# Optimization experiments

Measured on AMD Instinct MI355X. Metric: run time of the kernel, lower is better.

Reference implementation:

```python
import jax, jax.numpy as jnp
import numpy as np

NUM_HEADS = 16


def setup_inputs() -> dict:
    key = jax.random.key(0)
    k1, k2, k3 = jax.random.split(key, 3)
    T, B, E = 2048, 2, 1024
    query = jax.random.normal(k1, (T, B, E), dtype=jnp.float32)
    # xavier-uniform-ish init for qkv weight, small normal for output proj
    lim = (6.0 / (3 * E + E)) ** 0.5
    W_qkv = jax.random.uniform(k2, (3 * E, E), dtype=jnp.float32, minval=-lim, maxval=lim)
    W_o = jax.random.normal(k3, (E, E), dtype=jnp.float32) * 0.02
    b_qkv = jnp.zeros((3 * E,), dtype=jnp.float32)
    b_o = jnp.zeros((E,), dtype=jnp.float32)
    return {"query": query, "W_qkv": W_qkv, "b_qkv": b_qkv, "W_o": W_o, "b_o": b_o}


def reference(query, W_qkv, b_qkv, W_o, b_o):
    T, B, E = query.shape
    H = NUM_HEADS
    hd = E // H
    scaling = float(hd) ** -0.5

    # fused qkv projection: [T, B, 3E]
    qkv = jnp.einsum('tbe,fe->tbf', query, W_qkv) + b_qkv
    q, k, v = jnp.split(qkv, 3, axis=-1)
    q = q * scaling

    def to_heads(x):  # [T, B, E] -> [B*H, T, hd]
        return x.reshape(T, B * H, hd).transpose(1, 0, 2)

    q, k, v = to_heads(q), to_heads(k), to_heads(v)

    # explicit bmm QK^T -> softmax -> bmm AV (faithful to source)
    scores = jnp.einsum('bqd,bkd->bqk', q, k)          # [B*H, T, T]
    attn = jax.nn.softmax(scores, axis=-1)             # dropout p=0.0 (eval)
    ctx = jnp.einsum('bqk,bkd->bqd', attn, v)          # [B*H, T, hd]

    out = ctx.transpose(1, 0, 2).reshape(T, B, E)
    out = jnp.einsum('tbe,fe->tbf', out, W_o) + b_o    # o_net

    avg_weights = attn.reshape(B, H, T, T).sum(axis=1) / H  # need_weights=True path
    return out, avg_weights
```

## Files before the change

### kernel.cpp

```cpp
#include <hip/hip_runtime.h>
#include <stdint.h>

typedef unsigned short u16;
typedef __bf16 bf16x8 __attribute__((ext_vector_type(8)));
typedef float f32x4 __attribute__((ext_vector_type(4)));
typedef float f32x16 __attribute__((ext_vector_type(16)));

__device__ __forceinline__ u16 f2b(float f) {
  unsigned u = __builtin_bit_cast(unsigned, f);
  u += 0x7fffu + ((u >> 16) & 1u);
  return (u16)(u >> 16);
}

__device__ __forceinline__ float fexp2(float x) { return __builtin_amdgcn_exp2f(x); }

__device__ __forceinline__ void gld_lds16(const void* g, void* l) {
  __builtin_amdgcn_global_load_lds((const __attribute__((address_space(1))) unsigned int*)g,
                                   (__attribute__((address_space(3))) unsigned int*)l,
                                   16, 0, 0);
}

__global__ __launch_bounds__(256) void k_cvt3(
    const float* __restrict__ s0, u16* __restrict__ d0,
    const float* __restrict__ s1, u16* __restrict__ d1,
    const float* __restrict__ s2, u16* __restrict__ d2) {
  const int bx = blockIdx.x;
  const float* s;
  u16* d;
  int i0;
  if (bx < 4096)      { s = s0; d = d0; i0 = bx; }
  else if (bx < 7168) { s = s1; d = d1; i0 = bx - 4096; }
  else                { s = s2; d = d2; i0 = bx - 7168; }
  const int i = i0 * 256 + threadIdx.x;
  float4 v = reinterpret_cast<const float4*>(s)[i];
  ushort4 o;
  o.x = f2b(v.x); o.y = f2b(v.y); o.z = f2b(v.z); o.w = f2b(v.w);
  reinterpret_cast<ushort4*>(d)[i] = o;
}

template <int EPI>
__device__ __forceinline__ void gemm_body(
    const u16* __restrict__ A, const u16* __restrict__ B, const float* __restrict__ bias,
    float* __restrict__ outF, u16* __restrict__ q_ws, u16* __restrict__ k_ws,
    u16* __restrict__ vt_ws, int tm, int tn, u16* smem) {
  u16* Al0 = smem;
  u16* Bl0 = smem + 8192;
  const int tid = threadIdx.x;
  const int w = tid >> 6, lane = tid & 63;
  const int wr = w >> 1, wc = w & 1;
  const int lo = lane & 15, hi = lane >> 4;
  const size_t arow0 = (size_t)tm * 128;
  const size_t brow0 = (size_t)tn * 128;

  f32x4 acc[4][4] = {};

  const int rr = lane >> 2;
  const int kswz = ((lane & 3) ^ ((rr >> 1) & 3)) * 8;
  const int rsw = (lo >> 1) & 3;

  for (int rs = 0; rs < 2; ++rs) {
    int seg = rs * 4 + w;
    gld_lds16(A + (arow0 + seg * 16 + rr) * 1024 + kswz, &Al0[seg * 512 + lane * 8]);
    gld_lds16(B + (brow0 + seg * 16 + rr) * 1024 + kswz, &Bl0[seg * 512 + lane * 8]);
  }
  __syncthreads();
  int cur = 0;
  for (int kb = 0; kb < 32; ++kb) {
    if (kb + 1 < 32) {
      const int k0 = (kb + 1) * 32 + kswz;
      u16* Ad = Al0 + (cur ^ 1) * 4096;
      u16* Bd = Bl0 + (cur ^ 1) * 4096;
      for (int rs = 0; rs < 2; ++rs) {
        int seg = rs * 4 + w;
        gld_lds16(A + (arow0 + seg * 16 + rr) * 1024 + k0, &Ad[seg * 512 + lane * 8]);
        gld_lds16(B + (brow0 + seg * 16 + rr) * 1024 + k0, &Bd[seg * 512 + lane * 8]);
      }
    }
    const u16* Ac = Al0 + cur * 4096;
    const u16* Bc = Bl0 + cur * 4096;
    bf16x8 af[4], bfr[4];
#pragma unroll
    for (int m = 0; m < 4; ++m)
      af[m] = *(const bf16x8*)&Ac[(wr * 64 + m * 16 + lo) * 32 + ((hi ^ rsw) * 8)];
#pragma unroll
    for (int n = 0; n < 4; ++n)
      bfr[n] = *(const bf16x8*)&Bc[(wc * 64 + n * 16 + lo) * 32 + ((hi ^ rsw) * 8)];
#pragma unroll
    for (int m = 0; m < 4; ++m)
#pragma unroll
      for (int n = 0; n < 4; ++n)
        acc[m][n] = __builtin_amdgcn_mfma_f32_16x16x32_bf16(af[m], bfr[n], acc[m][n], 0, 0, 0);
    __syncthreads();
    cur ^= 1;
  }

  if (EPI == 0) {
#pragma unroll
    for (int n = 0; n < 4; ++n) {
      const int col = tn * 128 + wc * 64 + n * 16 + lo;
      const float bb = bias[col];
#pragma unroll
      for (int m = 0; m < 4; ++m)
#pragma unroll
        for (int r = 0; r < 4; ++r) {
          const int row = tm * 128 + wr * 64 + m * 16 + hi * 4 + r;
          outF[(size_t)row * 1024 + col] = acc[m][n][r] + bb;
        }
    }
  } else {
    const int sec = tn >> 3;
#pragma unroll
    for (int n = 0; n < 4; ++n) {
      const int cin = (tn & 7) * 128 + wc * 64 + n * 16 + lo;
      const int h = cin >> 6, d = cin & 63;
      const float bb = bias[sec * 1024 + cin];
#pragma unroll
      for (int m = 0; m < 4; ++m) {
        const int rowb = tm * 128 + wr * 64 + m * 16 + hi * 4;
        const int t0 = rowb >> 1;
        const float v0 = acc[m][n][0] + bb, v1 = acc[m][n][1] + bb;
        const float v2 = acc[m][n][2] + bb, v3 = acc[m][n][3] + bb;
        if (sec == 0) {
          const float s = 0.18033688f;
          q_ws[(((size_t)h * 2048 + t0) * 64) + d]            = f2b(v0 * s);
          q_ws[(((size_t)(16 + h) * 2048 + t0) * 64) + d]     = f2b(v1 * s);
          q_ws[(((size_t)h * 2048 + t0 + 1) * 64) + d]        = f2b(v2 * s);
          q_ws[(((size_t)(16 + h) * 2048 + t0 + 1) * 64) + d] = f2b(v3 * s);
        } else if (sec == 1) {
          k_ws[(((size_t)h * 2048 + t0) * 64) + d]            = f2b(v0);
          k_ws[(((size_t)(16 + h) * 2048 + t0) * 64) + d]     = f2b(v1);
          k_ws[(((size_t)h * 2048 + t0 + 1) * 64) + d]        = f2b(v2);
          k_ws[(((size_t)(16 + h) * 2048 + t0 + 1) * 64) + d] = f2b(v3);
        } else {
          const int tp0 = (t0 & ~12) | ((t0 & 4) << 1) | ((t0 & 8) >> 1);
          ushort2 p0, p1;
          p0.x = f2b(v0); p0.y = f2b(v2);
          p1.x = f2b(v1); p1.y = f2b(v3);
          *(ushort2*)(vt_ws + ((size_t)h * 64 + d) * 2048 + tp0) = p0;
          *(ushort2*)(vt_ws + ((size_t)(16 + h) * 64 + d) * 2048 + tp0) = p1;
        }
      }
    }
  }
}

__global__ __launch_bounds__(256) void k_gemm_qkv(
    const u16* __restrict__ A, const u16* __restrict__ B, const float* __restrict__ bias,
    u16* __restrict__ q_ws, u16* __restrict__ k_ws, u16* __restrict__ vt_ws) {
  __shared__ __align__(16) u16 smem[16384];
  const int flat = blockIdx.y * 24 + blockIdx.x;
  const int xcd = flat & 7, idx = flat >> 3;
  const int wg = xcd * 96 + idx;
  gemm_body<1>(A, B, bias, nullptr, q_ws, k_ws, vt_ws, wg / 24, wg % 24, smem);
}

__device__ __forceinline__ void avg_body(
    const u16* __restrict__ q_ws, const u16* __restrict__ k_ws,
    const float* __restrict__ c_ws, float* __restrict__ avg,
    int kx, int qy, int b, u16* smem) {
  u16* Kl0 = smem;
  const int tid = threadIdx.x, w = tid >> 6, lane = tid & 63;
  const int lo = lane & 15, hi = lane >> 4;
  const int kbase = kx * 128;
  const int qb = qy * 64;
  const int qrow = qb + w * 16 + lo;
  const int qrow_base = qb + w * 16 + hi * 4;

  const int r0 = tid >> 3, c0 = tid & 7;
  const int ldsoff = r0 * 128 + ((c0 ^ (r0 & 7)) << 4);
  const u16* kg = k_ws + ((size_t)(b * 16) * 2048 + kbase + r0) * 64 + c0 * 8;
  const int l7 = lo & 7;

  float acc[8][4] = {};
  const f32x4 zero = {0.f, 0.f, 0.f, 0.f};

  uint4 rg0 = *(const uint4*)(kg);
  uint4 rg1 = *(const uint4*)(kg + 32 * 64);
  uint4 rg2 = *(const uint4*)(kg + 64 * 64);
  uint4 rg3 = *(const uint4*)(kg + 96 * 64);
  {
    char* dst = (char*)Kl0 + ldsoff;
    *(uint4*)(dst) = rg0;
    *(uint4*)(dst + 32 * 128) = rg1;
    *(uint4*)(dst + 64 * 128) = rg2;
    *(uint4*)(dst + 96 * 128) = rg3;
  }
  __syncthreads();

  int cur = 0;
  for (int h = 0; h < 16; ++h) {
    const int bh = b * 16 + h;
    if (h + 1 < 16) {
      const u16* kgn = kg + (size_t)(h + 1) * 2048 * 64;
      rg0 = *(const uint4*)(kgn);
      rg1 = *(const uint4*)(kgn + 32 * 64);
      rg2 = *(const uint4*)(kgn + 64 * 64);
      rg3 = *(const uint4*)(kgn + 96 * 64);
    }
    const u16* qp = q_ws + ((size_t)bh * 2048 + qrow) * 64 + hi * 8;
    bf16x8 qf0 = *(const bf16x8*)qp;
    bf16x8 qf1 = *(const bf16x8*)(qp + 32);
    const float4 cf = *(const float4*)(c_ws + (size_t)bh * 2048 + qrow_base);
    const float cfa[4] = {cf.x, cf.y, cf.z, cf.w};
    const char* kbse = (const char*)(Kl0 + cur * 8192);
#pragma unroll
    for (int n = 0; n < 8; ++n) {
      const char* kp = kbse + (n * 16 + lo) * 128;
      bf16x8 k0 = *(const bf16x8*)(kp + ((hi ^ l7) << 4));
      bf16x8 k1 = *(const bf16x8*)(kp + (((hi + 4) ^ l7) << 4));
      f32x4 s = __builtin_amdgcn_mfma_f32_16x16x32_bf16(qf0, k0, zero, 0, 0, 0);
      s = __builtin_amdgcn_mfma_f32_16x16x32_bf16(qf1, k1, s, 0, 0, 0);
#pragma unroll
      for (int r = 0; r < 4; ++r) acc[n][r] += fexp2(s[r]) * cfa[r];
    }
    if (h + 1 < 16) {
      char* dst = (char*)(Kl0 + (cur ^ 1) * 8192) + ldsoff;
      *(uint4*)(dst) = rg0;
      *(uint4*)(dst + 32 * 128) = rg1;
      *(uint4*)(dst + 64 * 128) = rg2;
      *(uint4*)(dst + 96 * 128) = rg3;
      __syncthreads();
    }
    cur ^= 1;
  }

  const float s16 = 1.0f / 16.0f;
#pragma unroll
  for (int n = 0; n < 8; ++n)
#pragma unroll
    for (int r = 0; r < 4; ++r)
      avg[((size_t)(b * 2048 + qrow_base + r)) * 2048 + kbase + n * 16 + lo] = acc[n][r] * s16;
}

__global__ __launch_bounds__(256) void k_tail(
    const u16* __restrict__ ctx, const u16* __restrict__ wobf, const float* __restrict__ bo,
    float* __restrict__ out, const u16* __restrict__ q_ws, const u16* __restrict__ k_ws,
    const float* __restrict__ c_ws, float* __restrict__ avg) {
  __shared__ __align__(16) u16 smem[16384];
  const int bx = blockIdx.x;
  if (bx < 256) {
    gemm_body<0>(ctx, wobf, bo, out, nullptr, nullptr, nullptr, bx >> 3, bx & 7, smem);
  } else {
    const int id = bx - 256;
    avg_body(q_ws, k_ws, c_ws, avg, id & 15, (id >> 4) & 31, id >> 9, smem);
  }
}

__global__ __launch_bounds__(1024) void k_flash(
    const u16* __restrict__ q_ws, const u16* __restrict__ k_ws, const u16* __restrict__ vt_ws,
    u16* __restrict__ ctx_ws, float* __restrict__ c_ws) {
  __shared__ __align__(16) u16 KVl[33792];
  const int tid = threadIdx.x, w = tid >> 6, lane = tid & 63;
  const int h = lane >> 5, l31 = lane & 31, l7 = lane & 7;
  const int hh = w >> 3;
  const int wq = w & 7;
  const int tid_h = tid & 511;

  const int flat = blockIdx.y * 8 + blockIdx.x;
  const int xcd = flat & 7, idx = flat >> 3;
  const int bh = xcd * 4 + (idx & 3);
  const int qtile = idx >> 2;
  const int b = bh >> 4, head = bh & 15;
  const int qbase = qtile * 256;
  const int qrow = qbase + wq * 32 + l31;

  bf16x8 qf[4];
#pragma unroll
  for (int j = 0; j < 4; ++j)
    qf[j] = *(const bf16x8*)(q_ws + ((size_t)bh * 2048 + qrow) * 64 + j * 16 + h * 8);

  const int srow = tid_h >> 3, schk = tid_h & 7;
  const int xc = (schk ^ (srow & 7)) * 8;
  const u16* kgA = k_ws + ((size_t)bh * 2048 + hh * 1024 + srow) * 64 + xc;
  const u16* vgA = vt_ws + ((size_t)bh * 64 + srow) * 2048 + hh * 1024 + xc;

  f32x16 ca0 = {}, ca1 = {};
  float lrow = 0.f;

  {
    u16* base = KVl + hh * 8192;
    gld_lds16(kgA, base + tid_h * 8);
    gld_lds16(vgA, base + 4096 + tid_h * 8);
  }
  __syncthreads();

  int cur = 0;
  for (int it = 0; it < 16; ++it) {
    if (it < 15) {
      u16* base = KVl + (cur ^ 1) * 16384 + hh * 8192;
      gld_lds16(kgA + (size_t)(it + 1) * 4096, base + tid_h * 8);
      gld_lds16(vgA + (it + 1) * 64, base + 4096 + tid_h * 8);
    }
    const char* Kb = (const char*)(KVl + cur * 16384 + hh * 8192);
    const char* Vb = Kb + 8192;

    f32x16 st0 = {}, st1 = {};
    __builtin_amdgcn_s_setprio(1);
#pragma unroll
    for (int j = 0; j < 4; ++j) {
      bf16x8 k0 = *(const bf16x8*)(Kb + l31 * 128 + (((2 * j + h) ^ l7) * 16));
      bf16x8 k1 = *(const bf16x8*)(Kb + (32 + l31) * 128 + (((2 * j + h) ^ l7) * 16));
      st0 = __builtin_amdgcn_mfma_f32_32x32x16_bf16(k0, qf[j], st0, 0, 0, 0);
      st1 = __builtin_amdgcn_mfma_f32_32x32x16_bf16(k1, qf[j], st1, 0, 0, 0);
    }
    __builtin_amdgcn_s_setprio(0);

    float ps0 = 0.f, ps1 = 0.f;
#pragma unroll
    for (int r = 0; r < 16; ++r) { float p = fexp2(st0[r]); st0[r] = p; ps0 += p; }
#pragma unroll
    for (int r = 0; r < 16; ++r) { float p = fexp2(st1[r]); st1[r] = p; ps1 += p; }
    float ps = ps0 + ps1;
    ps += __shfl_xor(ps, 32, 64);
    lrow += ps;

    bf16x8 pb00, pb01, pb10, pb11;
#pragma unroll
    for (int i = 0; i < 8; ++i) {
      pb00[i] = (__bf16)st0[i];
      pb01[i] = (__bf16)st0[8 + i];
      pb10[i] = (__bf16)st1[i];
      pb11[i] = (__bf16)st1[8 + i];
    }

    __builtin_amdgcn_s_setprio(1);
#pragma unroll
    for (int t2 = 0; t2 < 2; ++t2)
#pragma unroll
      for (int kp = 0; kp < 2; ++kp) {
        const int ch = (4 * t2 + 2 * kp + h) ^ l7;
        bf16x8 v0 = *(const bf16x8*)(Vb + l31 * 128 + ch * 16);
        bf16x8 v1 = *(const bf16x8*)(Vb + (32 + l31) * 128 + ch * 16);
        const bf16x8 pv = (t2 == 0) ? (kp == 0 ? pb00 : pb01) : (kp == 0 ? pb10 : pb11);
        ca0 = __builtin_amdgcn_mfma_f32_32x32x16_bf16(v0, pv, ca0, 0, 0, 0);
        ca1 = __builtin_amdgcn_mfma_f32_32x32x16_bf16(v1, pv, ca1, 0, 0, 0);
      }
    __builtin_amdgcn_s_setprio(0);

    __syncthreads();
    cur ^= 1;
  }

  float* F = (float*)KVl;
  if (w >= 8) {
    const int g = w - 8;
#pragma unroll
    for (int r = 0; r < 16; ++r) {
      F[g * 2048 + r * 64 + lane] = ca0[r];
      F[g * 2048 + (16 + r) * 64 + lane] = ca1[r];
    }
    F[16384 + g * 64 + lane] = lrow;
  }
  __syncthreads();
  float inv = 0.f;
  if (w < 8) {
#pragma unroll
    for (int r = 0; r < 16; ++r) {
      ca0[r] += F[w * 2048 + r * 64 + lane];
      ca1[r] += F[w * 2048 + (16 + r) * 64 + lane];
    }
    lrow += F[16384 + w * 64 + lane];
    inv = 1.0f / lrow;
    if (lane < 32) c_ws[(size_t)bh * 2048 + qrow] = inv;
  }
  __syncthreads();
  u16* tw = KVl + w * 2048;
  if (w < 8) {
#pragma unroll
    for (int r = 0; r < 16; ++r) {
      const int d0 = (r & 3) + 8 * (r >> 2) + 4 * h;
      const int d1 = 32 + d0;
      *(u16*)((char*)tw + l31 * 128 + ((2 * d0) ^ (l7 << 4))) = f2b(ca0[r] * inv);
      *(u16*)((char*)tw + l31 * 128 + ((2 * d1) ^ (l7 << 4))) = f2b(ca1[r] * inv);
    }
  }
  __syncthreads();
  if (w < 8) {
#pragma unroll
    for (int it = 0; it < 4; ++it) {
      const int row = it * 8 + (lane >> 3);
      uint4 val = *(const uint4*)((const char*)tw + row * 128 + (((lane & 7) ^ (row & 7)) * 16));
      const int q = qbase + wq * 32 + row;
      *(uint4*)(ctx_ws + ((size_t)(q * 2 + b)) * 1024 + head * 64 + (lane & 7) * 8) = val;
    }
  }
}

extern "C" void kernel_launch(void* const* d_in, const int* in_sizes, int n_in,
                              void* d_out, int out_size, void* d_ws, size_t ws_size,
                              hipStream_t stream) {
  const float* query = (const float*)d_in[0];
  const float* Wqkv  = (const float*)d_in[1];
  const float* bqkv  = (const float*)d_in[2];
  const float* Wo    = (const float*)d_in[3];
  const float* bo    = (const float*)d_in[4];
  float* out = (float*)d_out;
  float* avg = out + (size_t)4096 * 1024;

  char* ws = (char*)d_ws;
  u16* qbf    = (u16*)(ws);
  u16* ctx_ws = (u16*)(ws);
  u16*   wqkvbf = (u16*)(ws + 8388608);
  float* c_ws   = (float*)(ws + 8388608);
  u16* wobf  = (u16*)(ws + 14680064);
  u16* q_ws  = (u16*)(ws + 16777216);
  u16* k_ws  = (u16*)(ws + 25165824);
  u16* vt_ws = (u16*)(ws + 33554432);

  k_cvt3<<<dim3(8192), dim3(256), 0, stream>>>(query, qbf, Wqkv, wqkvbf, Wo, wobf);
  k_gemm_qkv<<<dim3(24, 32), dim3(256), 0, stream>>>(
      qbf, wqkvbf, bqkv, q_ws, k_ws, vt_ws);
  k_flash<<<dim3(8, 32), dim3(1024), 0, stream>>>(
      q_ws, k_ws, vt_ws, ctx_ws, c_ws);
  k_tail<<<dim3(1280), dim3(256), 0, stream>>>(
      ctx_ws, wobf, bo, out, q_ws, k_ws, c_ws, avg);
}
```

Baseline: 140.0 us.

## Triple-buffer QKV GEMM loads, prefetch Q/c in avg pass, reorder tail blocks

Switches the QKV projection GEMM to a three-stage LDS ring buffer. It issues loads two k-tiles ahead and uses vmcnt-based waits with a single barrier per iteration, where the old loop had a double buffer and a trailing syncthreads. In the attention-average body, the Q fragments and softmax-normalizer values for the next head are now prefetched along with the K tile, hiding that global load latency. The tail kernel launches the avg blocks first and the output-projection GEMM blocks last, which changes how blocks are scheduled onto CUs. The cost is more LDS per QKV block, which may lower occupancy, plus extra registers for the prefetched fragments.

```diff
diff --git a/kernel.cpp b/kernel.cpp
--- a/kernel.cpp
+++ b/kernel.cpp
@@ -38,13 +38,13 @@
   reinterpret_cast<ushort4*>(d)[i] = o;
 }
 
-template <int EPI>
+template <int EPI, int TRIPLE>
 __device__ __forceinline__ void gemm_body(
     const u16* __restrict__ A, const u16* __restrict__ B, const float* __restrict__ bias,
     float* __restrict__ outF, u16* __restrict__ q_ws, u16* __restrict__ k_ws,
     u16* __restrict__ vt_ws, int tm, int tn, u16* smem) {
   u16* Al0 = smem;
-  u16* Bl0 = smem + 8192;
+  u16* Bl0 = smem + (TRIPLE ? 12288 : 8192);
   const int tid = threadIdx.x;
   const int w = tid >> 6, lane = tid & 63;
   const int wr = w >> 1, wc = w & 1;
@@ -58,41 +58,68 @@
   const int kswz = ((lane & 3) ^ ((rr >> 1) & 3)) * 8;
   const int rsw = (lo >> 1) & 3;
 
-  for (int rs = 0; rs < 2; ++rs) {
-    int seg = rs * 4 + w;
-    gld_lds16(A + (arow0 + seg * 16 + rr) * 1024 + kswz, &Al0[seg * 512 + lane * 8]);
-    gld_lds16(B + (brow0 + seg * 16 + rr) * 1024 + kswz, &Bl0[seg * 512 + lane * 8]);
-  }
-  __syncthreads();
-  int cur = 0;
-  for (int kb = 0; kb < 32; ++kb) {
-    if (kb + 1 < 32) {
-      const int k0 = (kb + 1) * 32 + kswz;
-      u16* Ad = Al0 + (cur ^ 1) * 4096;
-      u16* Bd = Bl0 + (cur ^ 1) * 4096;
-      for (int rs = 0; rs < 2; ++rs) {
-        int seg = rs * 4 + w;
-        gld_lds16(A + (arow0 + seg * 16 + rr) * 1024 + k0, &Ad[seg * 512 + lane * 8]);
-        gld_lds16(B + (brow0 + seg * 16 + rr) * 1024 + k0, &Bd[seg * 512 + lane * 8]);
-      }
-    }
-    const u16* Ac = Al0 + cur * 4096;
-    const u16* Bc = Bl0 + cur * 4096;
-    bf16x8 af[4], bfr[4];
-#pragma unroll
-    for (int m = 0; m < 4; ++m)
-      af[m] = *(const bf16x8*)&Ac[(wr * 64 + m * 16 + lo) * 32 + ((hi ^ rsw) * 8)];
-#pragma unroll
-    for (int n = 0; n < 4; ++n)
-      bfr[n] = *(const bf16x8*)&Bc[(wc * 64 + n * 16 + lo) * 32 + ((hi ^ rsw) * 8)];
-#pragma unroll
-    for (int m = 0; m < 4; ++m)
+#define GSTAGE(bufi, ktv)                                                          \
+  do {                                                                             \
+    const int koff_ = (ktv) * 32 + kswz;                                           \
+    u16* Ad_ = Al0 + (bufi) * 4096;                                                \
+    u16* Bd_ = Bl0 + (bufi) * 4096;                                                \
+    for (int rs_ = 0; rs_ < 2; ++rs_) {                                            \
+      int seg_ = rs_ * 4 + w;                                                      \
+      gld_lds16(A + (arow0 + seg_ * 16 + rr) * 1024 + koff_, &Ad_[seg_ * 512 + lane * 8]); \
+      gld_lds16(B + (brow0 + seg_ * 16 + rr) * 1024 + koff_, &Bd_[seg_ * 512 + lane * 8]); \
+    }                                                                              \
+  } while (0)
+
+  if (TRIPLE) {
+    GSTAGE(0, 0);
+    GSTAGE(1, 1);
+    for (int kt = 0; kt < 32; ++kt) {
+      if (kt < 31)
+        asm volatile("s_waitcnt vmcnt(4)\n\ts_barrier" ::: "memory");
+      else
+        asm volatile("s_waitcnt vmcnt(0)\n\ts_barrier" ::: "memory");
+      __builtin_amdgcn_sched_barrier(0);
+      if (kt + 2 < 32) GSTAGE((kt + 2) % 3, kt + 2);
+      const u16* Ac = Al0 + (kt % 3) * 4096;
+      const u16* Bc = Bl0 + (kt % 3) * 4096;
+      bf16x8 af[4], bfr[4];
+#pragma unroll
+      for (int m = 0; m < 4; ++m)
+        af[m] = *(const bf16x8*)&Ac[(wr * 64 + m * 16 + lo) * 32 + ((hi ^ rsw) * 8)];
 #pragma unroll
       for (int n = 0; n < 4; ++n)
-        acc[m][n] = __builtin_amdgcn_mfma_f32_16x16x32_bf16(af[m], bfr[n], acc[m][n], 0, 0, 0);
+        bfr[n] = *(const bf16x8*)&Bc[(wc * 64 + n * 16 + lo) * 32 + ((hi ^ rsw) * 8)];
+#pragma unroll
+      for (int m = 0; m < 4; ++m)
+#pragma unroll
+        for (int n = 0; n < 4; ++n)
+          acc[m][n] = __builtin_amdgcn_mfma_f32_16x16x32_bf16(af[m], bfr[n], acc[m][n], 0, 0, 0);
+    }
+  } else {
+    GSTAGE(0, 0);
     __syncthreads();
-    cur ^= 1;
-  }
+    int cur = 0;
+    for (int kb = 0; kb < 32; ++kb) {
+      if (kb + 1 < 32) GSTAGE(cur ^ 1, kb + 1);
+      const u16* Ac = Al0 + cur * 4096;
+      const u16* Bc = Bl0 + cur * 4096;
+      bf16x8 af[4], bfr[4];
+#pragma unroll
+      for (int m = 0; m < 4; ++m)
+        af[m] = *(const bf16x8*)&Ac[(wr * 64 + m * 16 + lo) * 32 + ((hi ^ rsw) * 8)];
+#pragma unroll
+      for (int n = 0; n < 4; ++n)
+        bfr[n] = *(const bf16x8*)&Bc[(wc * 64 + n * 16 + lo) * 32 + ((hi ^ rsw) * 8)];
+#pragma unroll
+      for (int m = 0; m < 4; ++m)
+#pragma unroll
+        for (int n = 0; n < 4; ++n)
+          acc[m][n] = __builtin_amdgcn_mfma_f32_16x16x32_bf16(af[m], bfr[n], acc[m][n], 0, 0, 0);
+      __syncthreads();
+      cur ^= 1;
+    }
+  }
+#undef GSTAGE
 
   if (EPI == 0) {
 #pragma unroll
@@ -147,11 +174,11 @@
 __global__ __launch_bounds__(256) void k_gemm_qkv(
     const u16* __restrict__ A, const u16* __restrict__ B, const float* __restrict__ bias,
     u16* __restrict__ q_ws, u16* __restrict__ k_ws, u16* __restrict__ vt_ws) {
-  __shared__ __align__(16) u16 smem[16384];
+  __shared__ __align__(16) u16 smem[24576];
   const int flat = blockIdx.y * 24 + blockIdx.x;
   const int xcd = flat & 7, idx = flat >> 3;
   const int wg = xcd * 96 + idx;
-  gemm_body<1>(A, B, bias, nullptr, q_ws, k_ws, vt_ws, wg / 24, wg % 24, smem);
+  gemm_body<1, 1>(A, B, bias, nullptr, q_ws, k_ws, vt_ws, wg / 24, wg % 24, smem);
 }
 
 __device__ __forceinline__ void avg_body(
@@ -185,22 +212,28 @@
     *(uint4*)(dst + 64 * 128) = rg2;
     *(uint4*)(dst + 96 * 128) = rg3;
   }
+  const u16* qp0 = q_ws + ((size_t)(b * 16) * 2048 + qrow) * 64 + hi * 8;
+  bf16x8 qf0 = *(const bf16x8*)qp0;
+  bf16x8 qf1 = *(const bf16x8*)(qp0 + 32);
+  float4 cf = *(const float4*)(c_ws + (size_t)(b * 16) * 2048 + qrow_base);
   __syncthreads();
 
   int cur = 0;
   for (int h = 0; h < 16; ++h) {
-    const int bh = b * 16 + h;
+    const int bhn = b * 16 + h + 1;
+    bf16x8 qf0n, qf1n;
+    float4 cfn;
     if (h + 1 < 16) {
       const u16* kgn = kg + (size_t)(h + 1) * 2048 * 64;
       rg0 = *(const uint4*)(kgn);
       rg1 = *(const uint4*)(kgn + 32 * 64);
       rg2 = *(const uint4*)(kgn + 64 * 64);
       rg3 = *(const uint4*)(kgn + 96 * 64);
-    }
-    const u16* qp = q_ws + ((size_t)bh * 2048 + qrow) * 64 + hi * 8;
-    bf16x8 qf0 = *(const bf16x8*)qp;
-    bf16x8 qf1 = *(const bf16x8*)(qp + 32);
-    const float4 cf = *(const float4*)(c_ws + (size_t)bh * 2048 + qrow_base);
+      const u16* qpn = q_ws + ((size_t)bhn * 2048 + qrow) * 64 + hi * 8;
+      qf0n = *(const bf16x8*)qpn;
+      qf1n = *(const bf16x8*)(qpn + 32);
+      cfn = *(const float4*)(c_ws + (size_t)bhn * 2048 + qrow_base);
+    }
     const float cfa[4] = {cf.x, cf.y, cf.z, cf.w};
     const char* kbse = (const char*)(Kl0 + cur * 8192);
 #pragma unroll
@@ -219,6 +252,7 @@
       *(uint4*)(dst + 32 * 128) = rg1;
       *(uint4*)(dst + 64 * 128) = rg2;
       *(uint4*)(dst + 96 * 128) = rg3;
+      qf0 = qf0n; qf1 = qf1n; cf = cfn;
       __syncthreads();
     }
     cur ^= 1;
@@ -238,11 +272,11 @@
     const float* __restrict__ c_ws, float* __restrict__ avg) {
   __shared__ __align__(16) u16 smem[16384];
   const int bx = blockIdx.x;
-  if (bx < 256) {
-    gemm_body<0>(ctx, wobf, bo, out, nullptr, nullptr, nullptr, bx >> 3, bx & 7, smem);
+  if (bx < 1024) {
+    avg_body(q_ws, k_ws, c_ws, avg, bx & 15, (bx >> 4) & 31, bx >> 9, smem);
   } else {
-    const int id = bx - 256;
-    avg_body(q_ws, k_ws, c_ws, avg, id & 15, (id >> 4) & 31, id >> 9, smem);
+    const int g = bx - 1024;
+    gemm_body<0, 0>(ctx, wobf, bo, out, nullptr, nullptr, nullptr, g >> 3, g & 7, smem);
   }
 }
 
```

After: 151.4 us. +8.1%, slower.

## Double query rows per avg block and load K tiles directly into LDS

Applied to the files above, without the earlier changes.

The attention-average part of the tail kernel now has each block cover 128 query rows instead of 64, so every K tile staged in LDS feeds twice as many MFMAs. This halves K reloads and the number of avg blocks, and the tail grid shrinks to match. K tiles are now loaded with global-to-LDS async loads with the swizzle applied on the global address, replacing the register round trip. The cost is doubled accumulator registers, which may lower occupancy, fewer blocks to fill the GPU, and a sync on every head iteration.

```diff
diff --git a/kernel.cpp b/kernel.cpp
--- a/kernel.cpp
+++ b/kernel.cpp
@@ -162,29 +162,21 @@
   const int tid = threadIdx.x, w = tid >> 6, lane = tid & 63;
   const int lo = lane & 15, hi = lane >> 4;
   const int kbase = kx * 128;
-  const int qb = qy * 64;
-  const int qrow = qb + w * 16 + lo;
-  const int qrow_base = qb + w * 16 + hi * 4;
+  const int qb = qy * 128;
+  const int qrow0 = qb + w * 32 + lo;
+  const int qrb0 = qb + w * 32 + hi * 4;
+  const int l7 = lo & 7;
 
   const int r0 = tid >> 3, c0 = tid & 7;
-  const int ldsoff = r0 * 128 + ((c0 ^ (r0 & 7)) << 4);
-  const u16* kg = k_ws + ((size_t)(b * 16) * 2048 + kbase + r0) * 64 + c0 * 8;
-  const int l7 = lo & 7;
-
-  float acc[8][4] = {};
+  const int xc = (c0 ^ (r0 & 7)) * 8;
+  const u16* kg = k_ws + ((size_t)(b * 16) * 2048 + kbase + r0) * 64 + xc;
+
+  float acc0[8][4] = {}, acc1[8][4] = {};
   const f32x4 zero = {0.f, 0.f, 0.f, 0.f};
 
-  uint4 rg0 = *(const uint4*)(kg);
-  uint4 rg1 = *(const uint4*)(kg + 32 * 64);
-  uint4 rg2 = *(const uint4*)(kg + 64 * 64);
-  uint4 rg3 = *(const uint4*)(kg + 96 * 64);
-  {
-    char* dst = (char*)Kl0 + ldsoff;
-    *(uint4*)(dst) = rg0;
-    *(uint4*)(dst + 32 * 128) = rg1;
-    *(uint4*)(dst + 64 * 128) = rg2;
-    *(uint4*)(dst + 96 * 128) = rg3;
-  }
+#pragma unroll
+  for (int j = 0; j < 4; ++j)
+    gld_lds16(kg + j * 32 * 64, Kl0 + (tid + 256 * j) * 8);
   __syncthreads();
 
   int cur = 0;
@@ -192,35 +184,38 @@
     const int bh = b * 16 + h;
     if (h + 1 < 16) {
       const u16* kgn = kg + (size_t)(h + 1) * 2048 * 64;
-      rg0 = *(const uint4*)(kgn);
-      rg1 = *(const uint4*)(kgn + 32 * 64);
-      rg2 = *(const uint4*)(kgn + 64 * 64);
-      rg3 = *(const uint4*)(kgn + 96 * 64);
-    }
-    const u16* qp = q_ws + ((size_t)bh * 2048 + qrow) * 64 + hi * 8;
-    bf16x8 qf0 = *(const bf16x8*)qp;
-    bf16x8 qf1 = *(const bf16x8*)(qp + 32);
-    const float4 cf = *(const float4*)(c_ws + (size_t)bh * 2048 + qrow_base);
-    const float cfa[4] = {cf.x, cf.y, cf.z, cf.w};
+      u16* dst = Kl0 + (cur ^ 1) * 8192;
+#pragma unroll
+      for (int j = 0; j < 4; ++j)
+        gld_lds16(kgn + j * 32 * 64, dst + (tid + 256 * j) * 8);
+    }
+    const u16* qp0 = q_ws + ((size_t)bh * 2048 + qrow0) * 64 + hi * 8;
+    bf16x8 qf00 = *(const bf16x8*)qp0;
+    bf16x8 qf01 = *(const bf16x8*)(qp0 + 32);
+    const u16* qp1 = qp0 + 16 * 64;
+    bf16x8 qf10 = *(const bf16x8*)qp1;
+    bf16x8 qf11 = *(const bf16x8*)(qp1 + 32);
+    const float4 cf0 = *(const float4*)(c_ws + (size_t)bh * 2048 + qrb0);
+    const float4 cf1 = *(const float4*)(c_ws + (size_t)bh * 2048 + qrb0 + 16);
+    const float c0a[4] = {cf0.x, cf0.y, cf0.z, cf0.w};
+    const float c1a[4] = {cf1.x, cf1.y, cf1.z, cf1.w};
     const char* kbse = (const char*)(Kl0 + cur * 8192);
 #pragma unroll
     for (int n = 0; n < 8; ++n) {
       const char* kp = kbse + (n * 16 + lo) * 128;
       bf16x8 k0 = *(const bf16x8*)(kp + ((hi ^ l7) << 4));
       bf16x8 k1 = *(const bf16x8*)(kp + (((hi + 4) ^ l7) << 4));
-      f32x4 s = __builtin_amdgcn_mfma_f32_16x16x32_bf16(qf0, k0, zero, 0, 0, 0);
-      s = __builtin_amdgcn_mfma_f32_16x16x32_bf16(qf1, k1, s, 0, 0, 0);
-#pragma unroll
-      for (int r = 0; r < 4; ++r) acc[n][r] += fexp2(s[r]) * cfa[r];
-    }
-    if (h + 1 < 16) {
-      char* dst = (char*)(Kl0 + (cur ^ 1) * 8192) + ldsoff;
-      *(uint4*)(dst) = rg0;
-      *(uint4*)(dst + 32 * 128) = rg1;
-      *(uint4*)(dst + 64 * 128) = rg2;
-      *(uint4*)(dst + 96 * 128) = rg3;
-      __syncthreads();
-    }
+      f32x4 s0 = __builtin_amdgcn_mfma_f32_16x16x32_bf16(qf00, k0, zero, 0, 0, 0);
+      s0 = __builtin_amdgcn_mfma_f32_16x16x32_bf16(qf01, k1, s0, 0, 0, 0);
+      f32x4 s1 = __builtin_amdgcn_mfma_f32_16x16x32_bf16(qf10, k0, zero, 0, 0, 0);
+      s1 = __builtin_amdgcn_mfma_f32_16x16x32_bf16(qf11, k1, s1, 0, 0, 0);
+#pragma unroll
+      for (int r = 0; r < 4; ++r) {
+        acc0[n][r] += fexp2(s0[r]) * c0a[r];
+        acc1[n][r] += fexp2(s1[r]) * c1a[r];
+      }
+    }
+    __syncthreads();
     cur ^= 1;
   }
 
@@ -228,8 +223,10 @@
 #pragma unroll
   for (int n = 0; n < 8; ++n)
 #pragma unroll
-    for (int r = 0; r < 4; ++r)
-      avg[((size_t)(b * 2048 + qrow_base + r)) * 2048 + kbase + n * 16 + lo] = acc[n][r] * s16;
+    for (int r = 0; r < 4; ++r) {
+      avg[((size_t)(b * 2048 + qrb0 + r)) * 2048 + kbase + n * 16 + lo] = acc0[n][r] * s16;
+      avg[((size_t)(b * 2048 + qrb0 + 16 + r)) * 2048 + kbase + n * 16 + lo] = acc1[n][r] * s16;
+    }
 }
 
 __global__ __launch_bounds__(256) void k_tail(
@@ -242,7 +239,7 @@
     gemm_body<0>(ctx, wobf, bo, out, nullptr, nullptr, nullptr, bx >> 3, bx & 7, smem);
   } else {
     const int id = bx - 256;
-    avg_body(q_ws, k_ws, c_ws, avg, id & 15, (id >> 4) & 31, id >> 9, smem);
+    avg_body(q_ws, k_ws, c_ws, avg, id & 15, (id >> 4) & 15, id >> 8, smem);
   }
 }
 
@@ -412,6 +409,6 @@
       qbf, wqkvbf, bqkv, q_ws, k_ws, vt_ws);
   k_flash<<<dim3(8, 32), dim3(1024), 0, stream>>>(
       q_ws, k_ws, vt_ws, ctx_ws, c_ws);
-  k_tail<<<dim3(1280), dim3(256), 0, stream>>>(
+  k_tail<<<dim3(768), dim3(256), 0, stream>>>(
       ctx_ws, wobf, bo, out, q_ws, k_ws, c_ws, avg);
 }
```

Result: slower. 149.8 us (+7.0%).
